# Performance work log

Measured on AMD Instinct MI355X. Metric: run time of the kernel, lower is better.

The kernel has to match this reference:

```python
import jax, jax.numpy as jnp
import numpy as np

N = 100000
E = 1600000
IN_FEATS = 256
HIDDEN = 128
CLASSES = 40

def _glorot(key, fan_in, fan_out):
    lim = float(np.sqrt(6.0 / (fan_in + fan_out)))
    return jax.random.uniform(key, (fan_in, fan_out), jnp.float32, -lim, lim)

def setup_inputs() -> dict:
    key = jax.random.key(0)
    ks = jax.random.split(key, 8)
    x = jax.random.normal(ks[0], (N, IN_FEATS), jnp.float32)
    src = jax.random.randint(ks[1], (E,), 0, N, jnp.int32)
    dst = jax.random.randint(ks[2], (E,), 0, N, jnp.int32)
    W0 = _glorot(ks[3], IN_FEATS, HIDDEN)
    b0 = jnp.zeros((HIDDEN,), jnp.float32)
    W1 = _glorot(ks[4], HIDDEN, HIDDEN)
    b1 = jnp.zeros((HIDDEN,), jnp.float32)
    Wc = _glorot(ks[5], HIDDEN, CLASSES)
    bc = jnp.zeros((CLASSES,), jnp.float32)
    return {"x": x, "src": src, "dst": dst, "W0": W0, "b0": b0,
            "W1": W1, "b1": b1, "Wc": Wc, "bc": bc}

def _degree_norms(src, dst, n):
    ones = jnp.ones(src.shape[0], jnp.float32)
    out_deg = jax.ops.segment_sum(ones, src, num_segments=n)
    in_deg = jax.ops.segment_sum(ones, dst, num_segments=n)
    c_src = jax.lax.rsqrt(jnp.maximum(out_deg, 1.0))  # D_out^{-1/2}
    c_dst = jax.lax.rsqrt(jnp.maximum(in_deg, 1.0))   # D_in^{-1/2}
    return c_src, c_dst

def _graph_conv(h, src, dst, c_src, c_dst, W, b, n):
    # transform first (cheaper when widths shrink), math-equivalent to DGL norm='both'
    h = h @ W
    h = h * c_src[:, None]
    agg = jax.ops.segment_sum(h[src], dst, num_segments=n)  # spmm gather/scatter
    return agg * c_dst[:, None] + b

def reference(x, src, dst, W0, b0, W1, b1, Wc, bc):
    n = x.shape[0]
    c_src, c_dst = _degree_norms(src, dst, n)
    h = _graph_conv(x, src, dst, c_src, c_dst, W0, b0, n)
    h = jax.nn.relu(h)  # dropout is identity at eval
    h = _graph_conv(h, src, dst, c_src, c_dst, W1, b1, n)
    logits = jax.nn.relu(h) @ Wc + bc
    return (h, logits)
```

## Files before the change

kernel.cpp:

```cpp
#include <hip/hip_runtime.h>
#include <cstdint>
#include <cstddef>


#define NPB 128
#define BSHIFT 7
#define NBLK_E 256

typedef __attribute__((ext_vector_type(8))) short short8;
typedef __attribute__((ext_vector_type(4))) float f32x4;

static __device__ __forceinline__ float4 ld4(const float* p) { return *(const float4*)p; }

static __device__ __forceinline__ float bf2f(unsigned int u) {
  union { unsigned int i; float f; } x; x.i = u << 16; return x.f;
}
static __device__ __forceinline__ unsigned int f2bf(float f) {
  union { float f; unsigned int i; } x; x.f = f;
  unsigned int r = x.i + 0x7fff + ((x.i >> 16) & 1);
  return r >> 16;
}

__global__ __launch_bounds__(256) void prep_weights(const float* __restrict__ W0,
                                                    const float* __restrict__ W1,
                                                    ushort* __restrict__ W0t,
                                                    ushort* __restrict__ W1t) {
  int t = blockIdx.x * 256 + threadIdx.x;
  if (t < 128 * 256) {
    int nn = t >> 8, kk = t & 255;
    W0t[nn * 256 + kk] = (ushort)f2bf(W0[kk * 128 + nn]);
  }
  if (t < 128 * 128) {
    int nn = t >> 7, kk = t & 127;
    W1t[nn * 128 + kk] = (ushort)f2bf(W1[kk * 128 + nn]);
  }
}

__global__ __launch_bounds__(256) void bucket_hist(const int* __restrict__ src,
                                                   const int* __restrict__ dst,
                                                   int* __restrict__ bhD, int* __restrict__ bhS,
                                                   int E, int nbk, int ept) {
  __shared__ int hD[1024], hS[1024];
  int t = threadIdx.x;
  for (int i = t; i < nbk; i += 256) { hD[i] = 0; hS[i] = 0; }
  __syncthreads();
  int base = blockIdx.x * 256 * ept + t;
  for (int j = 0; j < ept; j++) {
    int e = base + j * 256;
    if (e < E) {
      atomicAdd(&hD[dst[e] >> BSHIFT], 1);
      atomicAdd(&hS[src[e] >> BSHIFT], 1);
    }
  }
  __syncthreads();
  for (int i = t; i < nbk; i += 256) {
    bhD[(size_t)blockIdx.x * nbk + i] = hD[i];
    bhS[(size_t)blockIdx.x * nbk + i] = hS[i];
  }
}

__global__ __launch_bounds__(256) void bucket_scan_blocks(int* __restrict__ bhD,
                                                          int* __restrict__ bhS,
                                                          int* __restrict__ totD,
                                                          int* __restrict__ totS, int nbk) {
  __shared__ int lds[256];
  int b = blockIdx.x, t = threadIdx.x;
  int v = bhD[(size_t)t * nbk + b];
  lds[t] = v;
  __syncthreads();
  for (int off = 1; off < 256; off <<= 1) {
    int u = (t >= off) ? lds[t - off] : 0;
    __syncthreads();
    lds[t] += u;
    __syncthreads();
  }
  bhD[(size_t)t * nbk + b] = lds[t] - v;
  if (t == 255) totD[b] = lds[255];
  __syncthreads();
  int w = bhS[(size_t)t * nbk + b];
  lds[t] = w;
  __syncthreads();
  for (int off = 1; off < 256; off <<= 1) {
    int u = (t >= off) ? lds[t - off] : 0;
    __syncthreads();
    lds[t] += u;
    __syncthreads();
  }
  bhS[(size_t)t * nbk + b] = lds[t] - w;
  if (t == 255) totS[b] = lds[255];
}

__global__ __launch_bounds__(1024) void bucket_base(const int* __restrict__ totD,
                                                    const int* __restrict__ totS,
                                                    int* __restrict__ baseD,
                                                    int* __restrict__ baseS, int nbk) {
  __shared__ int lds[1024];
  int t = threadIdx.x;
  int v = (t < nbk) ? totD[t] : 0;
  lds[t] = v;
  __syncthreads();
  for (int off = 1; off < 1024; off <<= 1) {
    int u = (t >= off) ? lds[t - off] : 0;
    __syncthreads();
    lds[t] += u;
    __syncthreads();
  }
  if (t < nbk) baseD[t] = lds[t] - v;
  if (t == 1023) baseD[nbk] = lds[1023];
  __syncthreads();
  int w = (t < nbk) ? totS[t] : 0;
  lds[t] = w;
  __syncthreads();
  for (int off = 1; off < 1024; off <<= 1) {
    int u = (t >= off) ? lds[t - off] : 0;
    __syncthreads();
    lds[t] += u;
    __syncthreads();
  }
  if (t < nbk) baseS[t] = lds[t] - w;
  if (t == 1023) baseS[nbk] = lds[1023];
}

__global__ __launch_bounds__(256) void bucket_scatter(
    const int* __restrict__ src, const int* __restrict__ dst,
    const int* __restrict__ bhD, const int* __restrict__ bhS,
    const int* __restrict__ baseD, const int* __restrict__ baseS,
    unsigned int* __restrict__ ebufD, uint8_t* __restrict__ ebufS,
    int E, int nbk, int ept) {
  __shared__ int cD[1024], cS[1024];
  int k = blockIdx.x, t = threadIdx.x;
  for (int i = t; i < nbk; i += 256) {
    cD[i] = baseD[i] + bhD[(size_t)k * nbk + i];
    cS[i] = baseS[i] + bhS[(size_t)k * nbk + i];
  }
  __syncthreads();
  int base = k * 256 * ept + t;
  for (int j = 0; j < ept; j++) {
    int e = base + j * 256;
    if (e < E) {
      int s = src[e], d = dst[e];
      int pD = atomicAdd(&cD[d >> BSHIFT], 1);
      ebufD[pD] = ((unsigned int)(d & (NPB - 1)) << 17) | (unsigned int)s;
      int pS = atomicAdd(&cS[s >> BSHIFT], 1);
      ebufS[pS] = (uint8_t)(s & (NPB - 1));
    }
  }
}

__global__ __launch_bounds__(256) void csr_build(const unsigned int* __restrict__ ebufD,
                                                 const int* __restrict__ baseD,
                                                 int* __restrict__ row_start,
                                                 int* __restrict__ csr, int n, int nbk) {
  __shared__ int cnt[NPB], sc[NPB], cur[NPB];
  int b = blockIdx.x, t = threadIdx.x;
  if (t < NPB) cnt[t] = 0;
  __syncthreads();
  int s0 = baseD[b], s1 = baseD[b + 1];
  for (int i = s0 + t; i < s1; i += 256) atomicAdd(&cnt[ebufD[i] >> 17], 1);
  __syncthreads();
  int c = (t < NPB) ? cnt[t] : 0;
  if (t < NPB) sc[t] = c;
  __syncthreads();
  for (int off = 1; off < NPB; off <<= 1) {
    int u = (t < NPB && t >= off) ? sc[t - off] : 0;
    __syncthreads();
    if (t < NPB) sc[t] += u;
    __syncthreads();
  }
  if (t < NPB) {
    int start = s0 + sc[t] - c;
    cur[t] = start;
    int node = b * NPB + t;
    if (node < n) row_start[node] = start;
  }
  if (b == 0 && t == 0) row_start[n] = baseD[nbk];
  __syncthreads();
  for (int i = s0 + t; i < s1; i += 256) {
    unsigned int w = ebufD[i];
    int p = atomicAdd(&cur[w >> 17], 1);
    csr[p] = (int)(w & 0x1FFFFu);
  }
}

__global__ __launch_bounds__(256) void outdeg_norm(const uint8_t* __restrict__ ebufS,
                                                   const int* __restrict__ baseS,
                                                   float* __restrict__ c_src, int n) {
  __shared__ int cnt[NPB];
  int b = blockIdx.x, t = threadIdx.x;
  if (t < NPB) cnt[t] = 0;
  __syncthreads();
  int s0 = baseS[b], s1 = baseS[b + 1];
  for (int i = s0 + t; i < s1; i += 256) atomicAdd(&cnt[ebufS[i]], 1);
  __syncthreads();
  int node = b * NPB + t;
  if (t < NPB && node < n) c_src[node] = rsqrtf(fmaxf((float)cnt[t], 1.0f));
}


__global__ __launch_bounds__(256) void gemm256_mfma(const float* __restrict__ x,
                                                    const ushort* __restrict__ W0t,
                                                    const float* __restrict__ c_src,
                                                    ushort* __restrict__ t0b, int n) {
  __shared__ alignas(16) ushort As[64 * 64];
  __shared__ alignas(16) ushort Bs[128 * 64];
  int tid = threadIdx.x;
  int row0 = blockIdx.x * 64;
  int lane = tid & 63;
  int w = tid >> 6;
  int l16 = lane & 15, hi = lane >> 4;
  f32x4 acc[8];
#pragma unroll
  for (int c = 0; c < 8; c++) acc[c] = (f32x4){0.f, 0.f, 0.f, 0.f};

  for (int kt = 0; kt < 256; kt += 64) {
    {
      int r = tid >> 2;
      int gr = row0 + r;
#pragma unroll
      for (int u = 0; u < 2; u++) {
        int c8 = (tid & 3) * 2 + u;
        float4 v0 = make_float4(0.f, 0.f, 0.f, 0.f), v1 = v0;
        if (gr < n) {
          v0 = ld4(&x[(size_t)gr * 256 + kt + c8 * 8]);
          v1 = ld4(&x[(size_t)gr * 256 + kt + c8 * 8 + 4]);
        }
        uint4 o;
        o.x = f2bf(v0.x) | (f2bf(v0.y) << 16);
        o.y = f2bf(v0.z) | (f2bf(v0.w) << 16);
        o.z = f2bf(v1.x) | (f2bf(v1.y) << 16);
        o.w = f2bf(v1.z) | (f2bf(v1.w) << 16);
        *(uint4*)&As[r * 64 + (c8 ^ (r & 7)) * 8] = o;
      }
    }
    {
      int r = tid >> 1;
#pragma unroll
      for (int u = 0; u < 4; u++) {
        int c8 = (tid & 1) * 4 + u;
        uint4 o = *(const uint4*)&W0t[(size_t)r * 256 + kt + c8 * 8];
        *(uint4*)&Bs[r * 64 + (c8 ^ (r & 7)) * 8] = o;
      }
    }
    __syncthreads();
#pragma unroll
    for (int ks = 0; ks < 2; ks++) {
      int ar = w * 16 + l16;
      int ac = ks * 4 + hi;
      short8 a = *(const short8*)&As[ar * 64 + (ac ^ (ar & 7)) * 8];
#pragma unroll
      for (int c = 0; c < 8; c++) {
        int br = c * 16 + l16;
        short8 b = *(const short8*)&Bs[br * 64 + (ac ^ (br & 7)) * 8];
        acc[c] = __builtin_amdgcn_mfma_f32_16x16x32_bf16(a, b, acc[c], 0, 0, 0);
      }
    }
    __syncthreads();
  }
  float cs[4];
#pragma unroll
  for (int r = 0; r < 4; r++) {
    int gm = row0 + w * 16 + hi * 4 + r;
    cs[r] = (gm < n) ? c_src[gm] : 0.f;
  }
#pragma unroll
  for (int c = 0; c < 8; c++)
#pragma unroll
    for (int r = 0; r < 4; r++) {
      int gm = row0 + w * 16 + hi * 4 + r;
      if (gm < n) t0b[(size_t)gm * 128 + c * 16 + l16] = (ushort)f2bf(acc[c][r] * cs[r]);
    }
}

__global__ __launch_bounds__(256) void gemm128_mfma(const ushort* __restrict__ A,
                                                    const ushort* __restrict__ W1t,
                                                    const float* __restrict__ c_src,
                                                    ushort* __restrict__ Y, int n) {
  __shared__ alignas(16) ushort As[64 * 64];
  __shared__ alignas(16) ushort Bs[128 * 64];
  int tid = threadIdx.x;
  int row0 = blockIdx.x * 64;
  int lane = tid & 63;
  int w = tid >> 6;
  int l16 = lane & 15, hi = lane >> 4;
  f32x4 acc[8];
#pragma unroll
  for (int c = 0; c < 8; c++) acc[c] = (f32x4){0.f, 0.f, 0.f, 0.f};

  for (int kt = 0; kt < 128; kt += 64) {
    {
      int r = tid >> 2;
      int gr = row0 + r;
#pragma unroll
      for (int u = 0; u < 2; u++) {
        int c8 = (tid & 3) * 2 + u;
        uint4 o = make_uint4(0u, 0u, 0u, 0u);
        if (gr < n) o = *(const uint4*)&A[(size_t)gr * 128 + kt + c8 * 8];
        *(uint4*)&As[r * 64 + (c8 ^ (r & 7)) * 8] = o;
      }
    }
    {
      int r = tid >> 1;
#pragma unroll
      for (int u = 0; u < 4; u++) {
        int c8 = (tid & 1) * 4 + u;
        uint4 o = *(const uint4*)&W1t[(size_t)r * 128 + kt + c8 * 8];
        *(uint4*)&Bs[r * 64 + (c8 ^ (r & 7)) * 8] = o;
      }
    }
    __syncthreads();
#pragma unroll
    for (int ks = 0; ks < 2; ks++) {
      int ar = w * 16 + l16;
      int ac = ks * 4 + hi;
      short8 a = *(const short8*)&As[ar * 64 + (ac ^ (ar & 7)) * 8];
#pragma unroll
      for (int c = 0; c < 8; c++) {
        int br = c * 16 + l16;
        short8 b = *(const short8*)&Bs[br * 64 + (ac ^ (br & 7)) * 8];
        acc[c] = __builtin_amdgcn_mfma_f32_16x16x32_bf16(a, b, acc[c], 0, 0, 0);
      }
    }
    __syncthreads();
  }
  float cs[4];
#pragma unroll
  for (int r = 0; r < 4; r++) {
    int gm = row0 + w * 16 + hi * 4 + r;
    cs[r] = (gm < n) ? c_src[gm] : 0.f;
  }
#pragma unroll
  for (int c = 0; c < 8; c++)
#pragma unroll
    for (int r = 0; r < 4; r++) {
      int gm = row0 + w * 16 + hi * 4 + r;
      if (gm < n) Y[(size_t)gm * 128 + c * 16 + l16] = (ushort)f2bf(acc[c][r] * cs[r]);
    }
}

template <bool RELU, bool OUT_BF16>
__global__ __launch_bounds__(256) void agg_kernel(const ushort* __restrict__ T,
                                                  const int* __restrict__ row_start,
                                                  const int* __restrict__ csr_src,
                                                  const float* __restrict__ bias,
                                                  void* __restrict__ out, int n) {
  int lane = threadIdx.x & 63;
  int gw = (blockIdx.x * 256 + threadIdx.x) >> 6;
  int nw = gridDim.x * 4;
  float bx = bias[lane * 2], by = bias[lane * 2 + 1];
  for (int node = gw; node < n; node += nw) {
    int e0 = row_start[node], e1 = row_start[node + 1];
    float ax = 0.f, ay = 0.f;
    for (int eb = e0; eb < e1; eb += 64) {
      int rem = e1 - eb;
      int cnt = rem < 64 ? rem : 64;
      int msrc = (lane < rem) ? csr_src[eb + lane] : 0;
      int j = 0;
      for (; j + 7 < cnt; j += 8) {
        unsigned int w[8];
#pragma unroll
        for (int u = 0; u < 8; u++) {
          int s = __shfl(msrc, j + u);
          w[u] = *(const unsigned int*)&T[(size_t)s * 128 + lane * 2];
        }
#pragma unroll
        for (int u = 0; u < 8; u++) {
          ax += bf2f(w[u] & 0xffff);
          ay += bf2f(w[u] >> 16);
        }
      }
      for (; j + 1 < cnt; j += 2) {
        int s0 = __shfl(msrc, j), s1 = __shfl(msrc, j + 1);
        unsigned int w0 = *(const unsigned int*)&T[(size_t)s0 * 128 + lane * 2];
        unsigned int w1 = *(const unsigned int*)&T[(size_t)s1 * 128 + lane * 2];
        ax += bf2f(w0 & 0xffff) + bf2f(w1 & 0xffff);
        ay += bf2f(w0 >> 16) + bf2f(w1 >> 16);
      }
      if (j < cnt) {
        int s0 = __shfl(msrc, j);
        unsigned int w0 = *(const unsigned int*)&T[(size_t)s0 * 128 + lane * 2];
        ax += bf2f(w0 & 0xffff);
        ay += bf2f(w0 >> 16);
      }
    }
    float cd = rsqrtf(fmaxf((float)(e1 - e0), 1.0f));
    float rx = fmaf(ax, cd, bx);
    float ry = fmaf(ay, cd, by);
    if (RELU) { rx = fmaxf(rx, 0.f); ry = fmaxf(ry, 0.f); }
    if (OUT_BF16) {
      ((unsigned int*)out)[(size_t)node * 64 + lane] = f2bf(rx) | (f2bf(ry) << 16);
    } else {
      float2 r2; r2.x = rx; r2.y = ry;
      ((float2*)out)[(size_t)node * 64 + lane] = r2;
    }
  }
}

__global__ __launch_bounds__(256) void logits_kernel(const float* __restrict__ H,
                                                     const float* __restrict__ Wc,
                                                     const float* __restrict__ bc,
                                                     float* __restrict__ out, int n) {
  __shared__ float Wl[128 * 40];
  for (int i = threadIdx.x; i < 128 * 40; i += 256) Wl[i] = Wc[i];
  __syncthreads();
  int rl = threadIdx.x >> 3;
  int cg = threadIdx.x & 7;
  int r = blockIdx.x * 32 + rl;
  if (r >= n) return;
  float acc[5] = {0.f, 0.f, 0.f, 0.f, 0.f};
  const float* hr = &H[(size_t)r * 128];
  for (int k = 0; k < 128; k++) {
    float v = fmaxf(hr[k], 0.f);
#pragma unroll
    for (int j = 0; j < 5; j++) acc[j] = fmaf(v, Wl[k * 40 + cg * 5 + j], acc[j]);
  }
#pragma unroll
  for (int j = 0; j < 5; j++) out[(size_t)r * 40 + cg * 5 + j] = acc[j] + bc[cg * 5 + j];
}

extern "C" void kernel_launch(void* const* d_in, const int* in_sizes, int n_in,
                              void* d_out, int out_size, void* d_ws, size_t ws_size,
                              hipStream_t stream) {
  const float* x = (const float*)d_in[0];
  const int* src = (const int*)d_in[1];
  const int* dst = (const int*)d_in[2];
  const float* W0 = (const float*)d_in[3];
  const float* b0 = (const float*)d_in[4];
  const float* W1 = (const float*)d_in[5];
  const float* b1 = (const float*)d_in[6];
  const float* Wc = (const float*)d_in[7];
  const float* bc = (const float*)d_in[8];
  const int n = in_sizes[0] / 256;
  const int E = in_sizes[1];
  const int nbk = (n + NPB - 1) >> BSHIFT;
  const int ept = (E + NBLK_E * 256 - 1) / (NBLK_E * 256);

  char* wsp = (char*)d_ws;
  auto alloc = [&](size_t bytes) -> char* {
    char* p = wsp;
    wsp += (bytes + 255) & ~(size_t)255;
    return p;
  };
  ushort* t0b = (ushort*)alloc((size_t)n * 128 * sizeof(ushort));
  ushort* h1b = (ushort*)alloc((size_t)n * 128 * sizeof(ushort));
  float* c_src = (float*)alloc((size_t)n * sizeof(float));
  ushort* W0t = (ushort*)alloc((size_t)128 * 256 * sizeof(ushort));
  ushort* W1t = (ushort*)alloc((size_t)128 * 128 * sizeof(ushort));
  int* bhD = (int*)alloc((size_t)NBLK_E * nbk * sizeof(int));
  int* bhS = (int*)alloc((size_t)NBLK_E * nbk * sizeof(int));
  int* totD = (int*)alloc((size_t)nbk * sizeof(int));
  int* totS = (int*)alloc((size_t)nbk * sizeof(int));
  int* baseD = (int*)alloc((size_t)(nbk + 1) * sizeof(int));
  int* baseS = (int*)alloc((size_t)(nbk + 1) * sizeof(int));
  unsigned int* ebufD = (unsigned int*)alloc((size_t)E * sizeof(unsigned int));
  uint8_t* ebufS = (uint8_t*)alloc((size_t)E);
  int* row_start = (int*)alloc((size_t)(n + 1) * sizeof(int));
  int* csr = (int*)alloc((size_t)E * sizeof(int));

  float* h_out = (float*)d_out;
  float* logits = h_out + (size_t)n * 128;

  prep_weights<<<128, 256, 0, stream>>>(W0, W1, W0t, W1t);

  bucket_hist<<<NBLK_E, 256, 0, stream>>>(src, dst, bhD, bhS, E, nbk, ept);
  bucket_scan_blocks<<<nbk, 256, 0, stream>>>(bhD, bhS, totD, totS, nbk);
  bucket_base<<<1, 1024, 0, stream>>>(totD, totS, baseD, baseS, nbk);
  bucket_scatter<<<NBLK_E, 256, 0, stream>>>(src, dst, bhD, bhS, baseD, baseS,
                                             ebufD, ebufS, E, nbk, ept);
  csr_build<<<nbk, 256, 0, stream>>>(ebufD, baseD, row_start, csr, n, nbk);
  outdeg_norm<<<nbk, 256, 0, stream>>>(ebufS, baseS, c_src, n);

  gemm256_mfma<<<(n + 63) / 64, 256, 0, stream>>>(x, W0t, c_src, t0b, n);
  agg_kernel<true, true><<<2048, 256, 0, stream>>>(
      t0b, row_start, csr, b0, (void*)h1b, n);
  gemm128_mfma<<<(n + 63) / 64, 256, 0, stream>>>(h1b, W1t, c_src, t0b, n);
  agg_kernel<false, false><<<2048, 256, 0, stream>>>(
      t0b, row_start, csr, b1, (void*)h_out, n);
  logits_kernel<<<(n + 31) / 32, 256, 0, stream>>>(h_out, Wc, bc, logits, n);
}
```

Baseline: 460.9 us.

## Reorder layer-2 as aggregate-then-transform and fuse GEMM with logits; merge prep kernels

Layer 2 now aggregates the c_src-scaled ReLU output first (folded into the first aggregation's epilogue) and applies W1 afterwards. The W1 GEMM, bias, fp32 h output and the classifier logits are fused into one kernel that keeps the ReLU'd tile in LDS, so the separate logits pass no longer re-reads h from global memory. Weight prep is merged into the histogram kernel, the out-degree kernel is merged into CSR build, and edge blocks use a fixed chunk size, which cuts launch count. Exchanges: the logits now use a bf16-rounded ReLU(h), and the second aggregation result is rounded to bf16 before the GEMM.

```diff
diff --git a/kernel.cpp b/kernel.cpp
--- a/kernel.cpp
+++ b/kernel.cpp
@@ -5,7 +5,8 @@
 
 #define NPB 128
 #define BSHIFT 7
-#define NBLK_E 256
+#define EPT3 25
+#define CHUNK (EPT3 * 256)
 
 typedef __attribute__((ext_vector_type(8))) short short8;
 typedef __attribute__((ext_vector_type(4))) float f32x4;
@@ -21,31 +22,29 @@
   return r >> 16;
 }
 
-__global__ __launch_bounds__(256) void prep_weights(const float* __restrict__ W0,
-                                                    const float* __restrict__ W1,
-                                                    ushort* __restrict__ W0t,
-                                                    ushort* __restrict__ W1t) {
-  int t = blockIdx.x * 256 + threadIdx.x;
-  if (t < 128 * 256) {
-    int nn = t >> 8, kk = t & 255;
-    W0t[nn * 256 + kk] = (ushort)f2bf(W0[kk * 128 + nn]);
-  }
-  if (t < 128 * 128) {
-    int nn = t >> 7, kk = t & 127;
-    W1t[nn * 128 + kk] = (ushort)f2bf(W1[kk * 128 + nn]);
-  }
-}
-
-__global__ __launch_bounds__(256) void bucket_hist(const int* __restrict__ src,
-                                                   const int* __restrict__ dst,
-                                                   int* __restrict__ bhD, int* __restrict__ bhS,
-                                                   int E, int nbk, int ept) {
+__global__ __launch_bounds__(256) void hist_prep(
+    const int* __restrict__ src, const int* __restrict__ dst,
+    const float* __restrict__ W0, const float* __restrict__ W1,
+    ushort* __restrict__ W0t, ushort* __restrict__ W1t,
+    int* __restrict__ bhD, int* __restrict__ bhS, int E, int nbk, int nblk) {
   __shared__ int hD[1024], hS[1024];
-  int t = threadIdx.x;
+  int bid = blockIdx.x, t = threadIdx.x;
+  if (bid >= nblk) {
+    int idx = (bid - nblk) * 256 + t;
+    if (idx < 128 * 256) {
+      int nn = idx >> 8, kk = idx & 255;
+      W0t[nn * 256 + kk] = (ushort)f2bf(W0[kk * 128 + nn]);
+    }
+    if (idx < 128 * 128) {
+      int nn = idx >> 7, kk = idx & 127;
+      W1t[nn * 128 + kk] = (ushort)f2bf(W1[kk * 128 + nn]);
+    }
+    return;
+  }
   for (int i = t; i < nbk; i += 256) { hD[i] = 0; hS[i] = 0; }
   __syncthreads();
-  int base = blockIdx.x * 256 * ept + t;
-  for (int j = 0; j < ept; j++) {
+  int base = bid * CHUNK + t;
+  for (int j = 0; j < EPT3; j++) {
     int e = base + j * 256;
     if (e < E) {
       atomicAdd(&hD[dst[e] >> BSHIFT], 1);
@@ -54,18 +53,19 @@
   }
   __syncthreads();
   for (int i = t; i < nbk; i += 256) {
-    bhD[(size_t)blockIdx.x * nbk + i] = hD[i];
-    bhS[(size_t)blockIdx.x * nbk + i] = hS[i];
+    bhD[(size_t)bid * nbk + i] = hD[i];
+    bhS[(size_t)bid * nbk + i] = hS[i];
   }
 }
 
 __global__ __launch_bounds__(256) void bucket_scan_blocks(int* __restrict__ bhD,
                                                           int* __restrict__ bhS,
                                                           int* __restrict__ totD,
-                                                          int* __restrict__ totS, int nbk) {
+                                                          int* __restrict__ totS,
+                                                          int nbk, int nblk) {
   __shared__ int lds[256];
   int b = blockIdx.x, t = threadIdx.x;
-  int v = bhD[(size_t)t * nbk + b];
+  int v = (t < nblk) ? bhD[(size_t)t * nbk + b] : 0;
   lds[t] = v;
   __syncthreads();
   for (int off = 1; off < 256; off <<= 1) {
@@ -74,10 +74,10 @@
     lds[t] += u;
     __syncthreads();
   }
-  bhD[(size_t)t * nbk + b] = lds[t] - v;
+  if (t < nblk) bhD[(size_t)t * nbk + b] = lds[t] - v;
   if (t == 255) totD[b] = lds[255];
   __syncthreads();
-  int w = bhS[(size_t)t * nbk + b];
+  int w = (t < nblk) ? bhS[(size_t)t * nbk + b] : 0;
   lds[t] = w;
   __syncthreads();
   for (int off = 1; off < 256; off <<= 1) {
@@ -86,7 +86,7 @@
     lds[t] += u;
     __syncthreads();
   }
-  bhS[(size_t)t * nbk + b] = lds[t] - w;
+  if (t < nblk) bhS[(size_t)t * nbk + b] = lds[t] - w;
   if (t == 255) totS[b] = lds[255];
 }
 
@@ -126,7 +126,7 @@
     const int* __restrict__ bhD, const int* __restrict__ bhS,
     const int* __restrict__ baseD, const int* __restrict__ baseS,
     unsigned int* __restrict__ ebufD, uint8_t* __restrict__ ebufS,
-    int E, int nbk, int ept) {
+    int E, int nbk) {
   __shared__ int cD[1024], cS[1024];
   int k = blockIdx.x, t = threadIdx.x;
   for (int i = t; i < nbk; i += 256) {
@@ -134,8 +134,8 @@
     cS[i] = baseS[i] + bhS[(size_t)k * nbk + i];
   }
   __syncthreads();
-  int base = k * 256 * ept + t;
-  for (int j = 0; j < ept; j++) {
+  int base = k * CHUNK + t;
+  for (int j = 0; j < EPT3; j++) {
     int e = base + j * 256;
     if (e < E) {
       int s = src[e], d = dst[e];
@@ -147,16 +147,19 @@
   }
 }
 
-__global__ __launch_bounds__(256) void csr_build(const unsigned int* __restrict__ ebufD,
-                                                 const int* __restrict__ baseD,
-                                                 int* __restrict__ row_start,
-                                                 int* __restrict__ csr, int n, int nbk) {
-  __shared__ int cnt[NPB], sc[NPB], cur[NPB];
+__global__ __launch_bounds__(256) void csr_outdeg(
+    const unsigned int* __restrict__ ebufD, const uint8_t* __restrict__ ebufS,
+    const int* __restrict__ baseD, const int* __restrict__ baseS,
+    int* __restrict__ row_start, int* __restrict__ csr,
+    float* __restrict__ c_src, int n, int nbk) {
+  __shared__ int cnt[NPB], sc[NPB], cur[NPB], cntS[NPB];
   int b = blockIdx.x, t = threadIdx.x;
-  if (t < NPB) cnt[t] = 0;
+  if (t < NPB) { cnt[t] = 0; cntS[t] = 0; }
   __syncthreads();
   int s0 = baseD[b], s1 = baseD[b + 1];
   for (int i = s0 + t; i < s1; i += 256) atomicAdd(&cnt[ebufD[i] >> 17], 1);
+  int u0 = baseS[b], u1 = baseS[b + 1];
+  for (int i = u0 + t; i < u1; i += 256) atomicAdd(&cntS[ebufS[i]], 1);
   __syncthreads();
   int c = (t < NPB) ? cnt[t] : 0;
   if (t < NPB) sc[t] = c;
@@ -171,31 +174,19 @@
     int start = s0 + sc[t] - c;
     cur[t] = start;
     int node = b * NPB + t;
-    if (node < n) row_start[node] = start;
+    if (node < n) {
+      row_start[node] = start;
+      c_src[node] = rsqrtf(fmaxf((float)cntS[t], 1.0f));
+    }
   }
   if (b == 0 && t == 0) row_start[n] = baseD[nbk];
   __syncthreads();
   for (int i = s0 + t; i < s1; i += 256) {
-    unsigned int w = ebufD[i];
-    int p = atomicAdd(&cur[w >> 17], 1);
-    csr[p] = (int)(w & 0x1FFFFu);
-  }
-}
-
-__global__ __launch_bounds__(256) void outdeg_norm(const uint8_t* __restrict__ ebufS,
-                                                   const int* __restrict__ baseS,
-                                                   float* __restrict__ c_src, int n) {
-  __shared__ int cnt[NPB];
-  int b = blockIdx.x, t = threadIdx.x;
-  if (t < NPB) cnt[t] = 0;
-  __syncthreads();
-  int s0 = baseS[b], s1 = baseS[b + 1];
-  for (int i = s0 + t; i < s1; i += 256) atomicAdd(&cnt[ebufS[i]], 1);
-  __syncthreads();
-  int node = b * NPB + t;
-  if (t < NPB && node < n) c_src[node] = rsqrtf(fmaxf((float)cnt[t], 1.0f));
-}
-
+    unsigned int wv = ebufD[i];
+    int p = atomicAdd(&cur[wv >> 17], 1);
+    csr[p] = (int)(wv & 0x1FFFFu);
+  }
+}
 
 __global__ __launch_bounds__(256) void gemm256_mfma(const float* __restrict__ x,
                                                     const ushort* __restrict__ W0t,
@@ -271,82 +262,18 @@
     }
 }
 
-__global__ __launch_bounds__(256) void gemm128_mfma(const ushort* __restrict__ A,
-                                                    const ushort* __restrict__ W1t,
-                                                    const float* __restrict__ c_src,
-                                                    ushort* __restrict__ Y, int n) {
-  __shared__ alignas(16) ushort As[64 * 64];
-  __shared__ alignas(16) ushort Bs[128 * 64];
-  int tid = threadIdx.x;
-  int row0 = blockIdx.x * 64;
-  int lane = tid & 63;
-  int w = tid >> 6;
-  int l16 = lane & 15, hi = lane >> 4;
-  f32x4 acc[8];
-#pragma unroll
-  for (int c = 0; c < 8; c++) acc[c] = (f32x4){0.f, 0.f, 0.f, 0.f};
-
-  for (int kt = 0; kt < 128; kt += 64) {
-    {
-      int r = tid >> 2;
-      int gr = row0 + r;
-#pragma unroll
-      for (int u = 0; u < 2; u++) {
-        int c8 = (tid & 3) * 2 + u;
-        uint4 o = make_uint4(0u, 0u, 0u, 0u);
-        if (gr < n) o = *(const uint4*)&A[(size_t)gr * 128 + kt + c8 * 8];
-        *(uint4*)&As[r * 64 + (c8 ^ (r & 7)) * 8] = o;
-      }
-    }
-    {
-      int r = tid >> 1;
-#pragma unroll
-      for (int u = 0; u < 4; u++) {
-        int c8 = (tid & 1) * 4 + u;
-        uint4 o = *(const uint4*)&W1t[(size_t)r * 128 + kt + c8 * 8];
-        *(uint4*)&Bs[r * 64 + (c8 ^ (r & 7)) * 8] = o;
-      }
-    }
-    __syncthreads();
-#pragma unroll
-    for (int ks = 0; ks < 2; ks++) {
-      int ar = w * 16 + l16;
-      int ac = ks * 4 + hi;
-      short8 a = *(const short8*)&As[ar * 64 + (ac ^ (ar & 7)) * 8];
-#pragma unroll
-      for (int c = 0; c < 8; c++) {
-        int br = c * 16 + l16;
-        short8 b = *(const short8*)&Bs[br * 64 + (ac ^ (br & 7)) * 8];
-        acc[c] = __builtin_amdgcn_mfma_f32_16x16x32_bf16(a, b, acc[c], 0, 0, 0);
-      }
-    }
-    __syncthreads();
-  }
-  float cs[4];
-#pragma unroll
-  for (int r = 0; r < 4; r++) {
-    int gm = row0 + w * 16 + hi * 4 + r;
-    cs[r] = (gm < n) ? c_src[gm] : 0.f;
-  }
-#pragma unroll
-  for (int c = 0; c < 8; c++)
-#pragma unroll
-    for (int r = 0; r < 4; r++) {
-      int gm = row0 + w * 16 + hi * 4 + r;
-      if (gm < n) Y[(size_t)gm * 128 + c * 16 + l16] = (ushort)f2bf(acc[c][r] * cs[r]);
-    }
-}
-
-template <bool RELU, bool OUT_BF16>
+template <int MODE>
 __global__ __launch_bounds__(256) void agg_kernel(const ushort* __restrict__ T,
                                                   const int* __restrict__ row_start,
                                                   const int* __restrict__ csr_src,
+                                                  const float* __restrict__ c_src,
                                                   const float* __restrict__ bias,
-                                                  void* __restrict__ out, int n) {
+                                                  unsigned int* __restrict__ out, int n) {
   int lane = threadIdx.x & 63;
   int gw = (blockIdx.x * 256 + threadIdx.x) >> 6;
   int nw = gridDim.x * 4;
-  float bx = bias[lane * 2], by = bias[lane * 2 + 1];
+  float bx = 0.f, by = 0.f;
+  if (MODE == 0) { bx = bias[lane * 2]; by = bias[lane * 2 + 1]; }
   for (int node = gw; node < n; node += nw) {
     int e0 = row_start[node], e1 = row_start[node + 1];
     float ax = 0.f, ay = 0.f;
@@ -383,38 +310,110 @@
       }
     }
     float cd = rsqrtf(fmaxf((float)(e1 - e0), 1.0f));
-    float rx = fmaf(ax, cd, bx);
-    float ry = fmaf(ay, cd, by);
-    if (RELU) { rx = fmaxf(rx, 0.f); ry = fmaxf(ry, 0.f); }
-    if (OUT_BF16) {
-      ((unsigned int*)out)[(size_t)node * 64 + lane] = f2bf(rx) | (f2bf(ry) << 16);
+    float rx, ry;
+    if (MODE == 0) {
+      float csn = c_src[node];
+      rx = fmaxf(fmaf(ax, cd, bx), 0.f) * csn;
+      ry = fmaxf(fmaf(ay, cd, by), 0.f) * csn;
     } else {
-      float2 r2; r2.x = rx; r2.y = ry;
-      ((float2*)out)[(size_t)node * 64 + lane] = r2;
-    }
-  }
-}
-
-__global__ __launch_bounds__(256) void logits_kernel(const float* __restrict__ H,
-                                                     const float* __restrict__ Wc,
-                                                     const float* __restrict__ bc,
-                                                     float* __restrict__ out, int n) {
-  __shared__ float Wl[128 * 40];
-  for (int i = threadIdx.x; i < 128 * 40; i += 256) Wl[i] = Wc[i];
-  __syncthreads();
-  int rl = threadIdx.x >> 3;
-  int cg = threadIdx.x & 7;
-  int r = blockIdx.x * 32 + rl;
-  if (r >= n) return;
-  float acc[5] = {0.f, 0.f, 0.f, 0.f, 0.f};
-  const float* hr = &H[(size_t)r * 128];
-  for (int k = 0; k < 128; k++) {
-    float v = fmaxf(hr[k], 0.f);
-#pragma unroll
-    for (int j = 0; j < 5; j++) acc[j] = fmaf(v, Wl[k * 40 + cg * 5 + j], acc[j]);
-  }
-#pragma unroll
-  for (int j = 0; j < 5; j++) out[(size_t)r * 40 + cg * 5 + j] = acc[j] + bc[cg * 5 + j];
+      rx = ax * cd;
+      ry = ay * cd;
+    }
+    out[(size_t)node * 64 + lane] = f2bf(rx) | (f2bf(ry) << 16);
+  }
+}
+
+#define HSTRIDE 130
+__global__ __launch_bounds__(256) void final_kernel(const ushort* __restrict__ gb,
+                                                    const ushort* __restrict__ W1t,
+                                                    const float* __restrict__ b1,
+                                                    const float* __restrict__ Wc,
+                                                    const float* __restrict__ bc,
+                                                    float* __restrict__ h_out,
+                                                    float* __restrict__ logits, int n) {
+  __shared__ alignas(16) union {
+    struct { ushort As[64 * 64]; ushort Bs[128 * 64]; } g;
+    float Wl[128 * 40];
+  } sm;
+  __shared__ ushort Hs[64 * HSTRIDE];
+  int tid = threadIdx.x;
+  int row0 = blockIdx.x * 64;
+  int lane = tid & 63;
+  int w = tid >> 6;
+  int l16 = lane & 15, hi = lane >> 4;
+  f32x4 acc[8];
+#pragma unroll
+  for (int c = 0; c < 8; c++) acc[c] = (f32x4){0.f, 0.f, 0.f, 0.f};
+
+  for (int kt = 0; kt < 128; kt += 64) {
+    {
+      int r = tid >> 2;
+      int gr = row0 + r;
+#pragma unroll
+      for (int u = 0; u < 2; u++) {
+        int c8 = (tid & 3) * 2 + u;
+        uint4 o = make_uint4(0u, 0u, 0u, 0u);
+        if (gr < n) o = *(const uint4*)&gb[(size_t)gr * 128 + kt + c8 * 8];
+        *(uint4*)&sm.g.As[r * 64 + (c8 ^ (r & 7)) * 8] = o;
+      }
+    }
+    {
+      int r = tid >> 1;
+#pragma unroll
+      for (int u = 0; u < 4; u++) {
+        int c8 = (tid & 1) * 4 + u;
+        uint4 o = *(const uint4*)&W1t[(size_t)r * 128 + kt + c8 * 8];
+        *(uint4*)&sm.g.Bs[r * 64 + (c8 ^ (r & 7)) * 8] = o;
+      }
+    }
+    __syncthreads();
+#pragma unroll
+    for (int ks = 0; ks < 2; ks++) {
+      int ar = w * 16 + l16;
+      int ac = ks * 4 + hi;
+      short8 a = *(const short8*)&sm.g.As[ar * 64 + (ac ^ (ar & 7)) * 8];
+#pragma unroll
+      for (int c = 0; c < 8; c++) {
+        int br = c * 16 + l16;
+        short8 b = *(const short8*)&sm.g.Bs[br * 64 + (ac ^ (br & 7)) * 8];
+        acc[c] = __builtin_amdgcn_mfma_f32_16x16x32_bf16(a, b, acc[c], 0, 0, 0);
+      }
+    }
+    __syncthreads();
+  }
+#pragma unroll
+  for (int c = 0; c < 8; c++) {
+    int col = c * 16 + l16;
+    float bb = b1[col];
+#pragma unroll
+    for (int r = 0; r < 4; r++) {
+      int rl = w * 16 + hi * 4 + r;
+      int gm = row0 + rl;
+      float h2 = acc[c][r] + bb;
+      if (gm < n) h_out[(size_t)gm * 128 + col] = h2;
+      Hs[rl * HSTRIDE + col] = (ushort)f2bf(fmaxf(h2, 0.f));
+    }
+  }
+  __syncthreads();
+  for (int i = tid; i < 128 * 40; i += 256) sm.Wl[i] = Wc[i];
+  __syncthreads();
+  int cg = tid & 7;
+#pragma unroll
+  for (int pass = 0; pass < 2; pass++) {
+    int rl = pass * 32 + (tid >> 3);
+    int gm = row0 + rl;
+    if (gm < n) {
+      float a5[5] = {0.f, 0.f, 0.f, 0.f, 0.f};
+      for (int k = 0; k < 128; k++) {
+        float v = bf2f(Hs[rl * HSTRIDE + k]);
+#pragma unroll
+        for (int j = 0; j < 5; j++) a5[j] = fmaf(v, sm.Wl[k * 40 + cg * 5 + j], a5[j]);
+      }
+#pragma unroll
+      for (int j = 0; j < 5; j++)
+        logits[(size_t)gm * 40 + cg * 5 + j] = a5[j] + bc[cg * 5 + j];
+    }
+  }
 }
 
 extern "C" void kernel_launch(void* const* d_in, const int* in_sizes, int n_in,
@@ -432,7 +431,7 @@
   const int n = in_sizes[0] / 256;
   const int E = in_sizes[1];
   const int nbk = (n + NPB - 1) >> BSHIFT;
-  const int ept = (E + NBLK_E * 256 - 1) / (NBLK_E * 256);
+  const int nblk = (E + CHUNK - 1) / CHUNK;
 
   char* wsp = (char*)d_ws;
   auto alloc = [&](size_t bytes) -> char* {
@@ -441,12 +440,12 @@
     return p;
   };
   ushort* t0b = (ushort*)alloc((size_t)n * 128 * sizeof(ushort));
-  ushort* h1b = (ushort*)alloc((size_t)n * 128 * sizeof(ushort));
+  ushort* h1s = (ushort*)alloc((size_t)n * 128 * sizeof(ushort));
   float* c_src = (float*)alloc((size_t)n * sizeof(float));
   ushort* W0t = (ushort*)alloc((size_t)128 * 256 * sizeof(ushort));
   ushort* W1t = (ushort*)alloc((size_t)128 * 128 * sizeof(ushort));
-  int* bhD = (int*)alloc((size_t)NBLK_E * nbk * sizeof(int));
-  int* bhS = (int*)alloc((size_t)NBLK_E * nbk * sizeof(int));
+  int* bhD = (int*)alloc((size_t)nblk * nbk * sizeof(int));
+  int* bhS = (int*)alloc((size_t)nblk * nbk * sizeof(int));
   int* totD = (int*)alloc((size_t)nbk * sizeof(int));
   int* totS = (int*)alloc((size_t)nbk * sizeof(int));
   int* baseD = (int*)alloc((size_t)(nbk + 1) * sizeof(int));
@@ -459,21 +458,19 @@
   float* h_out = (float*)d_out;
   float* logits = h_out + (size_t)n * 128;
 
-  prep_weights<<<128, 256, 0, stream>>>(W0, W1, W0t, W1t);
-
-  bucket_hist<<<NBLK_E, 256, 0, stream>>>(src, dst, bhD, bhS, E, nbk, ept);
-  bucket_scan_blocks<<<nbk, 256, 0, stream>>>(bhD, bhS, totD, totS, nbk);
+  hist_prep<<<nblk + 128, 256, 0, stream>>>(src, dst, W0, W1, W0t, W1t,
+                                            bhD, bhS, E, nbk, nblk);
+  bucket_scan_blocks<<<nbk, 256, 0, stream>>>(bhD, bhS, totD, totS, nbk, nblk);
   bucket_base<<<1, 1024, 0, stream>>>(totD, totS, baseD, baseS, nbk);
-  bucket_scatter<<<NBLK_E, 256, 0, stream>>>(src, dst, bhD, bhS, baseD, baseS,
-                                             ebufD, ebufS, E, nbk, ept);
-  csr_build<<<nbk, 256, 0, stream>>>(ebufD, baseD, row_start, csr, n, nbk);
-  outdeg_norm<<<nbk, 256, 0, stream>>>(ebufS, baseS, c_src, n);
-
+  bucket_scatter<<<nblk, 256, 0, stream>>>(src, dst, bhD, bhS, baseD, baseS,
+                                           ebufD, ebufS, E, nbk);
+  csr_outdeg<<<nbk, 256, 0, stream>>>(ebufD, ebufS, baseD, baseS,
+                                      row_start, csr, c_src, n, nbk);
   gemm256_mfma<<<(n + 63) / 64, 256, 0, stream>>>(x, W0t, c_src, t0b, n);
-  agg_kernel<true, true><<<2048, 256, 0, stream>>>(
-      t0b, row_start, csr, b0, (void*)h1b, n);
-  gemm128_mfma<<<(n + 63) / 64, 256, 0, stream>>>(h1b, W1t, c_src, t0b, n);
-  agg_kernel<false, false><<<2048, 256, 0, stream>>>(
-      t0b, row_start, csr, b1, (void*)h_out, n);
-  logits_kernel<<<(n + 31) / 32, 256, 0, stream>>>(h_out, Wc, bc, logits, n);
-}
+  agg_kernel<0><<<2048, 256, 0, stream>>>(t0b, row_start, csr, c_src, b0,
+                                          (unsigned int*)h1s, n);
+  agg_kernel<1><<<2048, 256, 0, stream>>>(h1s, row_start, csr, c_src, b1,
+                                          (unsigned int*)t0b, n);
+  final_kernel<<<(n + 63) / 64, 256, 0, stream>>>(t0b, W1t, b1, Wc, bc,
+                                                  h_out, logits, n);
+}
```

Result: faster. 451.9 us (-2.0%).
